# Optimization experiments

Measured on AMD Instinct MI355X. Metric: run time of the kernel, lower is better.

Reference implementation:

```python
import jax, jax.numpy as jnp
import numpy as np

D_MODEL = 768
NUM_HEADS = 12
DEPTH = D_MODEL // NUM_HEADS


def setup_inputs() -> dict:
    key = jax.random.key(0)
    ks = jax.random.split(key, 11)
    B, S, D = 2, 2048, D_MODEL
    scale = 1.0 / np.sqrt(D)
    inp = {
        "v": jax.random.normal(ks[0], (B, S, D), jnp.float32),
        "k": jax.random.normal(ks[1], (B, S, D), jnp.float32),
        "q": jax.random.normal(ks[2], (B, S, D), jnp.float32),
        "wq": jax.random.normal(ks[3], (D, D), jnp.float32) * scale,
        "bq": jnp.zeros((D,), jnp.float32),
        "wk": jax.random.normal(ks[4], (D, D), jnp.float32) * scale,
        "bk": jnp.zeros((D,), jnp.float32),
        "wv": jax.random.normal(ks[5], (D, D), jnp.float32) * scale,
        "bv": jnp.zeros((D,), jnp.float32),
        "wo": jax.random.normal(ks[6], (D, D), jnp.float32) * scale,
        "bo": jnp.zeros((D,), jnp.float32),
    }
    return inp


def _split_heads(x):
    # (B, S, D) -> (B, H, S, depth)
    B, S, _ = x.shape
    return x.reshape(B, S, NUM_HEADS, DEPTH).transpose(0, 2, 1, 3)


def reference(v, k, q, wq, bq, wk, bk, wv, bv, wo, bo):
    B, S, D = q.shape
    qh = _split_heads(q @ wq + bq)  # (B,H,S,dh)
    kh = _split_heads(k @ wk + bk)
    vh = _split_heads(v @ wv + bv)
    logits = jnp.einsum("bhqd,bhkd->bhqk", qh, kh) / jnp.sqrt(
        jnp.asarray(DEPTH, qh.dtype)
    )
    attn = jax.nn.softmax(logits, axis=-1)  # (B,H,S,S)
    ctx = jnp.einsum("bhqk,bhkd->bhqd", attn, vh)
    ctx = ctx.transpose(0, 2, 1, 3).reshape(B, S, D)
    return ctx @ wo + bo
```

## Files before the change

kernel.cpp:

```cpp
#include <hip/hip_runtime.h>
#include <hip/hip_bf16.h>
#include <math.h>

typedef __bf16 bf16;
typedef __attribute__((ext_vector_type(8))) __bf16 bf16x8;
typedef __attribute__((ext_vector_type(4))) __bf16 bf16x4v;
typedef __attribute__((ext_vector_type(4))) float f32x4;
typedef __attribute__((ext_vector_type(2))) unsigned int u32x2;

#define MFMA16(a, b, c) __builtin_amdgcn_mfma_f32_16x16x32_bf16(a, b, c, 0, 0, 0)

__device__ __forceinline__ void gld16(const bf16* g, bf16* l) {
  __builtin_amdgcn_global_load_lds((const __attribute__((address_space(1))) void*)g,
                                   (__attribute__((address_space(3))) void*)l, 16, 0, 0);
}

__device__ __forceinline__ unsigned int pkbf(float a, float b) {
  union { unsigned int u; __bf16 h[2]; } r;
  r.h[0] = (bf16)a;
  r.h[1] = (bf16)b;
  return r.u;
}

__global__ __launch_bounds__(256) void prep(const float* __restrict__ q,
                                            const float* __restrict__ k,
                                            const float* __restrict__ v,
                                            bf16* __restrict__ qb, bf16* __restrict__ kb,
                                            bf16* __restrict__ vb,
                                            const float* __restrict__ w0,
                                            const float* __restrict__ w1,
                                            const float* __restrict__ w2,
                                            const float* __restrict__ w3,
                                            bf16* __restrict__ t0, bf16* __restrict__ t1,
                                            bf16* __restrict__ t2, bf16* __restrict__ t3) {
  const int lin = blockIdx.x;
  if (lin < 4608) {
    const int which = lin / 1536, idx = lin % 1536;
    const float* a = which == 0 ? q : (which == 1 ? k : v);
    bf16* o = which == 0 ? qb : (which == 1 ? kb : vb);
    const size_t i = ((size_t)idx * 256 + threadIdx.x) * 8;
    const float4 f0 = *(const float4*)(a + i);
    const float4 f1 = *(const float4*)(a + i + 4);
    bf16x8 r = {(bf16)f0.x, (bf16)f0.y, (bf16)f0.z, (bf16)f0.w,
                (bf16)f1.x, (bf16)f1.y, (bf16)f1.z, (bf16)f1.w};
    *(bf16x8*)(o + i) = r;
  } else {
    const int w = lin - 4608;
    const int z = w / 576, rem = w % 576;
    const int by = rem / 24, bx = rem % 24;
    const float* W = z == 0 ? w0 : (z == 1 ? w1 : (z == 2 ? w2 : w3));
    bf16* T = z == 0 ? t0 : (z == 1 ? t1 : (z == 2 ? t2 : t3));
    __shared__ float t[32][33];
    const int tx = threadIdx.x & 31, ty = threadIdx.x >> 5;
    const int c0 = bx * 32, r0 = by * 32;
#pragma unroll
    for (int i = 0; i < 4; ++i) {
      const int r = ty + 8 * i;
      t[r][tx] = W[(size_t)(r0 + r) * 768 + c0 + tx];
    }
    __syncthreads();
#pragma unroll
    for (int i = 0; i < 4; ++i) {
      const int r = ty + 8 * i;
      T[(size_t)(c0 + r) * 768 + r0 + tx] = (bf16)t[tx][r];
    }
  }
}

__device__ __forceinline__ void gemm_core(const bf16* __restrict__ A, const bf16* __restrict__ BT,
                                          int row0, int col0, bf16* As, bf16* Bs,
                                          f32x4 acc[4][4]) {
  const int tid = threadIdx.x;
  const int lane = tid & 63, wave = tid >> 6;
  const int m15 = lane & 15, kg = lane >> 4;
  const int wm = wave >> 1, wn = wave & 1;
  const int pr16 = lane & 15;
  const int pk8 = (lane >> 4) * 8;
#pragma unroll
  for (int i = 0; i < 4; ++i)
#pragma unroll
    for (int j = 0; j < 4; ++j) acc[i][j] = f32x4{0.f, 0.f, 0.f, 0.f};

  for (int k0 = 0; k0 < 768; k0 += 32) {
#pragma unroll
    for (int j = 0; j < 2; ++j) {
      const int i = wave * 2 + j;
      gld16(A + (size_t)(row0 + 16 * i + pr16) * 768 + k0 + pk8, As + i * 512);
      gld16(BT + (size_t)(col0 + 16 * i + pr16) * 768 + k0 + pk8, Bs + i * 512);
    }
    __syncthreads();
    bf16x8 af[4], bfr[4];
#pragma unroll
    for (int t = 0; t < 4; ++t)
      af[t] = *(const bf16x8*)(As + (4 * wm + t) * 512 + kg * 128 + m15 * 8);
#pragma unroll
    for (int t = 0; t < 4; ++t)
      bfr[t] = *(const bf16x8*)(Bs + (4 * wn + t) * 512 + kg * 128 + m15 * 8);
#pragma unroll
    for (int mt = 0; mt < 4; ++mt)
#pragma unroll
      for (int nt = 0; nt < 4; ++nt) acc[mt][nt] = MFMA16(af[mt], bfr[nt], acc[mt][nt]);
    __syncthreads();
  }
}

__global__ __launch_bounds__(256, 3) void gemm_qkv(
    const bf16* __restrict__ qb, const bf16* __restrict__ kb, const bf16* __restrict__ vb,
    const bf16* __restrict__ wqT, const bf16* __restrict__ wkT, const bf16* __restrict__ wvT,
    const float* __restrict__ bq, const float* __restrict__ bk, const float* __restrict__ bv,
    bf16* __restrict__ Qh, bf16* __restrict__ Kh, bf16* __restrict__ Vt) {
  __shared__ bf16 As[128 * 32], Bs[128 * 32];
  const bf16 *A, *BT;
  const float* bias;
  bf16* out;
  int mode;
  if (blockIdx.z == 0) { A = qb; BT = wqT; bias = bq; out = Qh; mode = 0; }
  else if (blockIdx.z == 1) { A = kb; BT = wkT; bias = bk; out = Kh; mode = 0; }
  else { A = vb; BT = wvT; bias = bv; out = Vt; mode = 1; }
  const int row0 = blockIdx.y * 128, col0 = blockIdx.x * 128;
  f32x4 acc[4][4];
  gemm_core(A, BT, row0, col0, As, Bs, acc);

  const int lane = threadIdx.x & 63, wave = threadIdx.x >> 6;
  const int m15 = lane & 15, kg = lane >> 4;
  const int wm = wave >> 1, wn = wave & 1;
#pragma unroll
  for (int mt = 0; mt < 4; ++mt) {
#pragma unroll
    for (int nt = 0; nt < 4; ++nt) {
      const int col = col0 + 64 * wn + 16 * nt + m15;
      const float bb = bias[col];
      const int h = col >> 6, d = col & 63;
      const int rowb = row0 + 64 * wm + 16 * mt + kg * 4;
      const int b = rowb >> 11, s0 = rowb & 2047;
      if (mode == 0) {
#pragma unroll
        for (int r = 0; r < 4; ++r)
          out[((size_t)(b * 12 + h) * 2048 + s0 + r) * 64 + d] = (bf16)(acc[mt][nt][r] + bb);
      } else {
        bf16x4v pk;
#pragma unroll
        for (int r = 0; r < 4; ++r) pk[r] = (bf16)(acc[mt][nt][r] + bb);
        *(bf16x4v*)&out[((size_t)(b * 12 + h) * 64 + d) * 2048 + s0] = pk;
      }
    }
  }
}

__global__ __launch_bounds__(256, 3) void gemm_out(const bf16* __restrict__ A,
                                                   const bf16* __restrict__ BT,
                                                   const float* __restrict__ bias,
                                                   float* __restrict__ out) {
  __shared__ bf16 As[128 * 32], Bs[128 * 32];
  const int row0 = blockIdx.y * 128, col0 = blockIdx.x * 128;
  f32x4 acc[4][4];
  gemm_core(A, BT, row0, col0, As, Bs, acc);

  const int lane = threadIdx.x & 63, wave = threadIdx.x >> 6;
  const int m15 = lane & 15, kg = lane >> 4;
  const int wm = wave >> 1, wn = wave & 1;
#pragma unroll
  for (int mt = 0; mt < 4; ++mt) {
#pragma unroll
    for (int nt = 0; nt < 4; ++nt) {
      const int col = col0 + 64 * wn + 16 * nt + m15;
      const float bb = bias[col];
      const int rowb = row0 + 64 * wm + 16 * mt + kg * 4;
#pragma unroll
      for (int r = 0; r < 4; ++r)
        out[(size_t)(rowb + r) * 768 + col] = acc[mt][nt][r] + bb;
    }
  }
}

__global__ __launch_bounds__(512, 6) void attn_kernel(const bf16* __restrict__ Q,
                                                      const bf16* __restrict__ K,
                                                      const bf16* __restrict__ VT,
                                                      bf16* __restrict__ ctx) {
  __shared__ __align__(16) bf16 S[21504];

  const int tid = threadIdx.x;
  const int lane = tid & 63, wave = tid >> 6;
  const int m15 = lane & 15, kg = lane >> 4;
  const int lin = blockIdx.x;
  const int bh = lin % 24, qblk = lin / 24;
  const size_t hb = (size_t)bh * 2048 * 64;
  const bf16* Qp = Q + hb;
  const bf16* Kp = K + hb;
  const bf16* Vp = VT + hb;
  const int pipe = wave >> 2;
  const int qrow0 = qblk * 64 + (wave & 3) * 16;
  bf16* Pw = S + 16384 + wave * 640;

  const int kpr = lane & 7, kpc = (lane >> 3) * 8;
  const int vpr = lane & 15, vpc = (lane >> 4) * 8;

  bf16x8 qf[2];
#pragma unroll
  for (int ks = 0; ks < 2; ++ks) {
    bf16x8 tv = *(const bf16x8*)&Qp[(size_t)(qrow0 + m15) * 64 + 32 * ks + kg * 8];
#pragma unroll
    for (int j = 0; j < 8; ++j) tv[j] = (bf16)((float)tv[j] * 0.125f);
    qf[ks] = tv;
  }

  f32x4 o[4];
  float lpq = 0.f;
#pragma unroll
  for (int nt = 0; nt < 4; ++nt) o[nt] = f32x4{0.f, 0.f, 0.f, 0.f};

#pragma unroll
  for (int j = 0; j < 2; ++j) {
    const int idx = wave * 2 + j;
    const int sp = idx >> 3, r8 = idx & 7;
    const int kc = sp * 1024;
    if (r8 < 4)
      gld16(Kp + (size_t)(kc + 8 * r8 + kpr) * 64 + kpc, S + sp * 2 * 2048 + r8 * 512);
    else {
      const int i = r8 - 4;
      gld16(Vp + (size_t)(16 * i + vpr) * 2048 + kc + vpc, S + 8192 + sp * 2 * 2048 + i * 512);
    }
  }

  for (int c = 0; c < 32; ++c) {
    const int buf = c & 1;
    __syncthreads();
    if (c < 31) {
      const int nb = buf ^ 1;
#pragma unroll
      for (int j = 0; j < 2; ++j) {
        const int idx = wave * 2 + j;
        const int sp = idx >> 3, r8 = idx & 7;
        const int kc = sp * 1024 + (c + 1) * 32;
        if (r8 < 4)
          gld16(Kp + (size_t)(kc + 8 * r8 + kpr) * 64 + kpc,
                S + (sp * 2 + nb) * 2048 + r8 * 512);
        else {
          const int i = r8 - 4;
          gld16(Vp + (size_t)(16 * i + vpr) * 2048 + kc + vpc,
                S + 8192 + (sp * 2 + nb) * 2048 + i * 512);
        }
      }
    }
    const bf16* KsB = S + (pipe * 2 + buf) * 2048;
    const bf16* VsB = S + 8192 + (pipe * 2 + buf) * 2048;

    f32x4 s[2];
#pragma unroll
    for (int kt = 0; kt < 2; ++kt) s[kt] = f32x4{0.f, 0.f, 0.f, 0.f};
#pragma unroll
    for (int ks = 0; ks < 2; ++ks) {
#pragma unroll
      for (int kt = 0; kt < 2; ++kt) {
        const int key = 16 * kt + m15;
        const bf16x8 kf =
            *(const bf16x8*)&KsB[(key >> 3) * 512 + (4 * ks + kg) * 64 + (key & 7) * 8];
        s[kt] = MFMA16(kf, qf[ks], s[kt]);
      }
    }
#pragma unroll
    for (int kt = 0; kt < 2; ++kt) {
      float pe0 = __expf(s[kt][0]);
      float pe1 = __expf(s[kt][1]);
      float pe2 = __expf(s[kt][2]);
      float pe3 = __expf(s[kt][3]);
      lpq += (pe0 + pe1) + (pe2 + pe3);
      u32x2 pk;
      pk[0] = pkbf(pe0, pe1);
      pk[1] = pkbf(pe2, pe3);
      *(u32x2*)&Pw[m15 * 40 + kt * 16 + kg * 4] = pk;
    }
    asm volatile("s_waitcnt lgkmcnt(0)" ::: "memory");
    const bf16x8 pf = *(const bf16x8*)&Pw[m15 * 40 + kg * 8];
#pragma unroll
    for (int nt = 0; nt < 4; ++nt) {
      const int d = 16 * nt + m15;
      const bf16x8 vf =
          *(const bf16x8*)&VsB[(d >> 4) * 512 + kg * 128 + (d & 15) * 8];
      o[nt] = MFMA16(pf, vf, o[nt]);
    }
  }

  lpq += __shfl_xor(lpq, 16);
  lpq += __shfl_xor(lpq, 32);

  __syncthreads();
  float* sc = (float*)S;
  if (wave >= 4) {
    const int rg = (wave - 4) * 1088;
#pragma unroll
    for (int nt = 0; nt < 4; ++nt) *(f32x4*)&sc[rg + nt * 256 + lane * 4] = o[nt];
    sc[rg + 1024 + lane] = lpq;
  }
  __syncthreads();
  if (wave < 4) {
    const int rg = wave * 1088;
#pragma unroll
    for (int nt = 0; nt < 4; ++nt) {
      const f32x4 po = *(const f32x4*)&sc[rg + nt * 256 + lane * 4];
#pragma unroll
      for (int j = 0; j < 4; ++j) o[nt][j] += po[j];
    }
    lpq += sc[rg + 1024 + lane];
    float lpr[4];
#pragma unroll
    for (int r = 0; r < 4; ++r) lpr[r] = __shfl(lpq, kg * 4 + r);
    const int b = bh / 12, h = bh % 12;
#pragma unroll
    for (int nt = 0; nt < 4; ++nt)
#pragma unroll
      for (int r = 0; r < 4; ++r) {
        const int sr = qrow0 + kg * 4 + r;
        ctx[((size_t)(b * 2048) + sr) * 768 + h * 64 + 16 * nt + m15] =
            (bf16)(o[nt][r] / lpr[r]);
      }
  }
}

extern "C" void kernel_launch(void* const* d_in, const int* in_sizes, int n_in,
                              void* d_out, int out_size, void* d_ws, size_t ws_size,
                              hipStream_t stream) {
  const float* v = (const float*)d_in[0];
  const float* k = (const float*)d_in[1];
  const float* q = (const float*)d_in[2];
  const float* wq = (const float*)d_in[3];
  const float* bq = (const float*)d_in[4];
  const float* wk = (const float*)d_in[5];
  const float* bk = (const float*)d_in[6];
  const float* wv = (const float*)d_in[7];
  const float* bv = (const float*)d_in[8];
  const float* wo = (const float*)d_in[9];
  const float* bo = (const float*)d_in[10];

  char* ws = (char*)d_ws;
  const size_t SEG = (size_t)4096 * 768 * sizeof(bf16);
  const size_t WSEG = (size_t)768 * 768 * sizeof(bf16);
  bf16* Qh = (bf16*)(ws + 0 * SEG);
  bf16* Kh = (bf16*)(ws + 1 * SEG);
  bf16* Vt = (bf16*)(ws + 2 * SEG);
  bf16* qb = (bf16*)(ws + 3 * SEG);
  bf16* kb = (bf16*)(ws + 4 * SEG);
  bf16* vb = (bf16*)(ws + 5 * SEG);
  bf16* ctx = qb;
  bf16* wqT = (bf16*)(ws + 6 * SEG);
  bf16* wkT = (bf16*)(ws + 6 * SEG + WSEG);
  bf16* wvT = (bf16*)(ws + 6 * SEG + 2 * WSEG);
  bf16* woT = (bf16*)(ws + 6 * SEG + 3 * WSEG);

  prep<<<dim3(6912), 256, 0, stream>>>(q, k, v, qb, kb, vb, wq, wk, wv, wo,
                                       wqT, wkT, wvT, woT);
  gemm_qkv<<<dim3(6, 32, 3), 256, 0, stream>>>(qb, kb, vb, wqT, wkT, wvT, bq, bk, bv,
                                               Qh, Kh, Vt);
  attn_kernel<<<dim3(768), 512, 0, stream>>>(Qh, Kh, Vt, ctx);
  gemm_out<<<dim3(6, 32), 256, 0, stream>>>(ctx, woT, bo, (float*)d_out);
}
```

Before: 217.6 us.

## Issue next K/V tile loads before waiting and use partial vmcnt waits

```diff
diff --git a/kernel.cpp b/kernel.cpp
--- a/kernel.cpp
+++ b/kernel.cpp
@@ -194,6 +194,25 @@
 
   const int kpr = lane & 7, kpc = (lane >> 3) * 8;
   const int vpr = lane & 15, vpc = (lane >> 4) * 8;
+  const int r8a = (2 * wave) & 7;
+  const int sp = wave >> 2;
+  const bf16 *srcA, *srcB;
+  bf16 *dstA, *dstB;
+  int cstep;
+  if (r8a < 4) {
+    srcA = Kp + (size_t)(sp * 1024 + 8 * r8a + kpr) * 64 + kpc;
+    srcB = srcA + 8 * 64;
+    dstA = S + sp * 4096 + r8a * 512;
+    dstB = dstA + 512;
+    cstep = 32 * 64;
+  } else {
+    const int ia = r8a - 4;
+    srcA = Vp + (size_t)(16 * ia + vpr) * 2048 + sp * 1024 + vpc;
+    srcB = srcA + 16 * 2048;
+    dstA = S + 8192 + sp * 4096 + ia * 512;
+    dstB = dstA + 512;
+    cstep = 32;
+  }
 
   bf16x8 qf[2];
 #pragma unroll
@@ -209,39 +228,27 @@
 #pragma unroll
   for (int nt = 0; nt < 4; ++nt) o[nt] = f32x4{0.f, 0.f, 0.f, 0.f};
 
-#pragma unroll
-  for (int j = 0; j < 2; ++j) {
-    const int idx = wave * 2 + j;
-    const int sp = idx >> 3, r8 = idx & 7;
-    const int kc = sp * 1024;
-    if (r8 < 4)
-      gld16(Kp + (size_t)(kc + 8 * r8 + kpr) * 64 + kpc, S + sp * 2 * 2048 + r8 * 512);
-    else {
-      const int i = r8 - 4;
-      gld16(Vp + (size_t)(16 * i + vpr) * 2048 + kc + vpc, S + 8192 + sp * 2 * 2048 + i * 512);
-    }
-  }
+  gld16(srcA, dstA);
+  gld16(srcB, dstB);
+  srcA += cstep;
+  srcB += cstep;
 
   for (int c = 0; c < 32; ++c) {
     const int buf = c & 1;
-    __syncthreads();
+    if (c) __builtin_amdgcn_s_barrier();
     if (c < 31) {
-      const int nb = buf ^ 1;
-#pragma unroll
-      for (int j = 0; j < 2; ++j) {
-        const int idx = wave * 2 + j;
-        const int sp = idx >> 3, r8 = idx & 7;
-        const int kc = sp * 1024 + (c + 1) * 32;
-        if (r8 < 4)
-          gld16(Kp + (size_t)(kc + 8 * r8 + kpr) * 64 + kpc,
-                S + (sp * 2 + nb) * 2048 + r8 * 512);
-        else {
-          const int i = r8 - 4;
-          gld16(Vp + (size_t)(16 * i + vpr) * 2048 + kc + vpc,
-                S + 8192 + (sp * 2 + nb) * 2048 + i * 512);
-        }
-      }
-    }
+      const int nb = (buf ^ 1) * 2048;
+      gld16(srcA, dstA + nb);
+      gld16(srcB, dstB + nb);
+      srcA += cstep;
+      srcB += cstep;
+      asm volatile("s_waitcnt vmcnt(2)" ::: "memory");
+    } else {
+      asm volatile("s_waitcnt vmcnt(0)" ::: "memory");
+    }
+    __builtin_amdgcn_sched_barrier(0);
+    __builtin_amdgcn_s_barrier();
+
     const bf16* KsB = S + (pipe * 2 + buf) * 2048;
     const bf16* VsB = S + 8192 + (pipe * 2 + buf) * 2048;
 
```

New measurement: 219.3 us. Within noise of the previous version (+0.8%).
